# Optimization experiments

Hardware: AMD Instinct MI355X
Metric: run time of the kernel (lower is better)

Reference implementation:

```python
import jax, jax.numpy as jnp
import numpy as np

H = 64  # hidden size
T_ENC = 20
T_DEC = 30


def setup_inputs() -> dict:
    key = jax.random.key(0)
    ks = jax.random.split(key, 12)
    B = 65536
    s = 0.1
    return {
        "input_traj": jax.random.normal(ks[0], (B, T_ENC, 2), jnp.float32),
        "W_ih_enc": jax.random.normal(ks[1], (4 * H, 2), jnp.float32) * s,
        "W_hh_enc": jax.random.normal(ks[2], (4 * H, H), jnp.float32) * s,
        "b_ih_enc": jax.random.normal(ks[3], (4 * H,), jnp.float32) * s,
        "b_hh_enc": jax.random.normal(ks[4], (4 * H,), jnp.float32) * s,
        "W_ih_dec": jax.random.normal(ks[5], (4 * H, H), jnp.float32) * s,
        "W_hh_dec": jax.random.normal(ks[6], (4 * H, H), jnp.float32) * s,
        "b_ih_dec": jax.random.normal(ks[7], (4 * H,), jnp.float32) * s,
        "b_hh_dec": jax.random.normal(ks[8], (4 * H,), jnp.float32) * s,
        "W_emb": jax.random.normal(ks[9], (2, H), jnp.float32) * s,
        "b_emb": jax.random.normal(ks[10], (2,), jnp.float32) * s,
    }


def _lstm_cell(x, h, c, Wih, Whh, bih, bhh):
    # PyTorch LSTMCell gate order: i, f, g, o
    gates = x @ Wih.T + bih + h @ Whh.T + bhh  # [B, 4H]
    i, f, g, o = jnp.split(gates, 4, axis=-1)
    i = jax.nn.sigmoid(i)
    f = jax.nn.sigmoid(f)
    g = jnp.tanh(g)
    o = jax.nn.sigmoid(o)
    c_new = f * c + i * g
    h_new = o * jnp.tanh(c_new)
    return h_new, c_new


def reference(input_traj, W_ih_enc, W_hh_enc, b_ih_enc, b_hh_enc,
              W_ih_dec, W_hh_dec, b_ih_dec, b_hh_dec, W_emb, b_emb):
    B = input_traj.shape[0]
    h0 = jnp.zeros((B, H), input_traj.dtype)
    c0 = jnp.zeros((B, H), input_traj.dtype)

    # Encoder: scan over 20 timesteps (time-major inputs)
    xs = jnp.transpose(input_traj, (1, 0, 2))  # [T_ENC, B, 2]

    def enc_step(carry, x_t):
        h, c = carry
        h, c = _lstm_cell(x_t, h, c, W_ih_enc, W_hh_enc, b_ih_enc, b_hh_enc)
        return (h, c), None

    (h, c), _ = jax.lax.scan(enc_step, (h0, c0), xs)

    # Decoder: 30 steps, input at each step is the current hidden state
    def dec_step(carry, _):
        h, c = carry
        h, c = _lstm_cell(h, h, c, W_ih_dec, W_hh_dec, b_ih_dec, b_hh_dec)
        pos = h @ W_emb.T + b_emb  # [B, 2]
        return (h, c), pos

    (_, _), pos_seq = jax.lax.scan(dec_step, (h, c), None, length=T_DEC)
    pred_traj = jnp.transpose(pos_seq, (1, 0, 2))  # [B, T_DEC, 2]
    return pred_traj
```

## Files before the change

kernel.cpp:

```cpp
#include <hip/hip_runtime.h>

#define T_ENC 20
#define T_DEC 30
#define WAVES 4
#define EPB (WAVES * 32)

typedef __attribute__((ext_vector_type(8))) short short8;
typedef __attribute__((ext_vector_type(16))) float f32x16;

#if __has_builtin(__builtin_amdgcn_exp2f)
#define EXP2F(x) __builtin_amdgcn_exp2f(x)
#else
#define EXP2F(x) exp2f(x)
#endif
#if __has_builtin(__builtin_amdgcn_rcpf)
#define RCPF(x) __builtin_amdgcn_rcpf(x)
#else
#define RCPF(x) (1.0f / (x))
#endif

__device__ __forceinline__ float fast_sigmoid(float x) {
  float e = EXP2F(-1.4426950408889634f * x);
  return RCPF(1.0f + e);
}
__device__ __forceinline__ float fast_tanh(float x) {
  float e = EXP2F(2.8853900817779268f * x);
  return 1.0f - 2.0f * RCPF(e + 1.0f);
}

__device__ __forceinline__ unsigned short f2bf(float f) {
  unsigned u = __float_as_uint(f);
  u += 0x7fffu + ((u >> 16) & 1u);
  return (unsigned short)(u >> 16);
}
__device__ __forceinline__ float bf2f(unsigned short b) {
  return __uint_as_float(((unsigned)b) << 16);
}

#define MFMA32(a, b, c) __builtin_amdgcn_mfma_f32_32x32x16_bf16(a, b, c, 0, 0, 0)

__global__ __launch_bounds__(256, 1)
void SinglePrediction_88493506167138_kernel(
    const float* __restrict__ x,
    const float* __restrict__ W_ih_enc,
    const float* __restrict__ W_hh_enc,
    const float* __restrict__ b_ih_enc,
    const float* __restrict__ b_hh_enc,
    const float* __restrict__ W_ih_dec,
    const float* __restrict__ W_hh_dec,
    const float* __restrict__ b_ih_dec,
    const float* __restrict__ b_hh_dec,
    const float* __restrict__ W_emb,
    const float* __restrict__ b_emb,
    float* __restrict__ out)
{
  __shared__ __align__(16) unsigned short Wbf[2][256 * 64];
  __shared__ __align__(16) unsigned short hT[WAVES][2][32 * 64];
  __shared__ __align__(16) float xlds[WAVES][32][T_ENC * 2];
  __shared__ float bsum_l[256];

  const int tid = threadIdx.x;
  const int lane = tid & 63;
  const int wid = tid >> 6;
  const int hi5 = lane >> 5;
  const int l31 = lane & 31;
  const int beb = blockIdx.x * EPB;

  {
    const float4* src = (const float4*)(x + (size_t)beb * (T_ENC * 2));
    float4* dst = (float4*)&xlds[0][0][0];
    for (int i = tid; i < EPB * T_ENC * 2 / 4; i += 256) dst[i] = src[i];
  }
  for (int i = tid; i < 256 * 64; i += 256) {
    int row = i >> 6, k = i & 63;
    float w = W_hh_enc[i];
    unsigned short hb = f2bf(w);
    unsigned short lb = f2bf(w - bf2f(hb));
    int si = (row << 6) | (k ^ ((row & 7) << 3));
    Wbf[0][si] = hb;
    Wbf[1][si] = lb;
  }
  bsum_l[tid] = b_ih_enc[tid] + b_hh_enc[tid];
  {
    float4 z = {0.f, 0.f, 0.f, 0.f};
    float4* p = (float4*)&hT[wid][0][0];
    for (int i = lane; i < 512; i += 64) p[i] = z;
  }
  __syncthreads();

  float biasv[8], wi0[8], wi1[8];
#pragma unroll
  for (int nt = 0; nt < 8; nt++) {
    int n = nt * 32 + l31;
    biasv[nt] = bsum_l[n];
    float2 wv = *(const float2*)&W_ih_enc[2 * n];
    wi0[nt] = wv.x;
    wi1[nt] = wv.y;
  }

  float c01[2][16];
#pragma unroll
  for (int p = 0; p < 2; p++)
#pragma unroll
    for (int q = 0; q < 16; q++) c01[p][q] = 0.f;

  const int sw = (l31 & 7) << 3;
  const int kbase = hi5 << 3;

#pragma unroll 1
  for (int t = 0; t < T_ENC; t++) {
    short8 ah[4], al[4];
#pragma unroll
    for (int kt = 0; kt < 4; kt++) {
      int sk = (kt * 16 + kbase) ^ sw;
      ah[kt] = *(const short8*)&hT[wid][0][(l31 << 6) + sk];
      al[kt] = *(const short8*)&hT[wid][1][(l31 << 6) + sk];
    }
    float2 xr[16];
#pragma unroll
    for (int q = 0; q < 16; q++) {
      int row = (q & 3) + 8 * (q >> 2) + 4 * hi5;
      xr[q] = *(const float2*)&xlds[wid][row][2 * t];
    }
    f32x16 acc[8];
#pragma unroll
    for (int nt = 0; nt < 8; nt++)
#pragma unroll
      for (int q = 0; q < 16; q++)
        acc[nt][q] = fmaf(xr[q].x, wi0[nt], fmaf(xr[q].y, wi1[nt], biasv[nt]));
#pragma unroll
    for (int kt = 0; kt < 4; kt++) {
      short8 bh[8], bl[8];
      int sk = (kt * 16 + kbase) ^ sw;
#pragma unroll
      for (int nt = 0; nt < 8; nt++) {
        int r = nt * 32 + l31;
        bh[nt] = *(const short8*)&Wbf[0][(r << 6) + sk];
        bl[nt] = *(const short8*)&Wbf[1][(r << 6) + sk];
      }
#pragma unroll
      for (int nt = 0; nt < 8; nt++) acc[nt] = MFMA32(ah[kt], bh[nt], acc[nt]);
#pragma unroll
      for (int nt = 0; nt < 8; nt++) acc[nt] = MFMA32(al[kt], bh[nt], acc[nt]);
#pragma unroll
      for (int nt = 0; nt < 8; nt++) acc[nt] = MFMA32(ah[kt], bl[nt], acc[nt]);
    }
#pragma unroll
    for (int p = 0; p < 2; p++)
#pragma unroll
      for (int q = 0; q < 16; q++) {
        float ig = fast_sigmoid(acc[0 + p][q]);
        float fg = fast_sigmoid(acc[2 + p][q]);
        float gg = fast_tanh(acc[4 + p][q]);
        float og = fast_sigmoid(acc[6 + p][q]);
        float cn = fmaf(fg, c01[p][q], ig * gg);
        c01[p][q] = cn;
        float hn = og * fast_tanh(cn);
        unsigned short hb = f2bf(hn);
        unsigned short lb = f2bf(hn - bf2f(hb));
        int row = (q & 3) + 8 * (q >> 2) + 4 * hi5;
        int col = l31 + 32 * p;
        int si = (row << 6) | (col ^ ((row & 7) << 3));
        hT[wid][0][si] = hb;
        hT[wid][1][si] = lb;
      }
  }

  __syncthreads();
  for (int i = tid; i < 256 * 64; i += 256) {
    int row = i >> 6, k = i & 63;
    float w = W_ih_dec[i] + W_hh_dec[i];
    unsigned short hb = f2bf(w);
    unsigned short lb = f2bf(w - bf2f(hb));
    int si = (row << 6) | (k ^ ((row & 7) << 3));
    Wbf[0][si] = hb;
    Wbf[1][si] = lb;
  }
  bsum_l[tid] = b_ih_dec[tid] + b_hh_dec[tid];
  __syncthreads();

#pragma unroll
  for (int nt = 0; nt < 8; nt++) biasv[nt] = bsum_l[nt * 32 + l31];
  const float we00 = W_emb[l31];
  const float we01 = W_emb[32 + l31];
  const float we10 = W_emb[64 + l31];
  const float we11 = W_emb[96 + l31];
  const float be0 = b_emb[0];
  const float be1 = b_emb[1];

#pragma unroll 1
  for (int t = 0; t < T_DEC; t++) {
    short8 ah[4], al[4];
#pragma unroll
    for (int kt = 0; kt < 4; kt++) {
      int sk = (kt * 16 + kbase) ^ sw;
      ah[kt] = *(const short8*)&hT[wid][0][(l31 << 6) + sk];
      al[kt] = *(const short8*)&hT[wid][1][(l31 << 6) + sk];
    }
    f32x16 acc[8];
#pragma unroll
    for (int nt = 0; nt < 8; nt++)
#pragma unroll
      for (int q = 0; q < 16; q++) acc[nt][q] = biasv[nt];
#pragma unroll
    for (int kt = 0; kt < 4; kt++) {
      short8 bh[8], bl[8];
      int sk = (kt * 16 + kbase) ^ sw;
#pragma unroll
      for (int nt = 0; nt < 8; nt++) {
        int r = nt * 32 + l31;
        bh[nt] = *(const short8*)&Wbf[0][(r << 6) + sk];
        bl[nt] = *(const short8*)&Wbf[1][(r << 6) + sk];
      }
#pragma unroll
      for (int nt = 0; nt < 8; nt++) acc[nt] = MFMA32(ah[kt], bh[nt], acc[nt]);
#pragma unroll
      for (int nt = 0; nt < 8; nt++) acc[nt] = MFMA32(al[kt], bh[nt], acc[nt]);
#pragma unroll
      for (int nt = 0; nt < 8; nt++) acc[nt] = MFMA32(ah[kt], bl[nt], acc[nt]);
    }
    float hs[2][16];
#pragma unroll
    for (int p = 0; p < 2; p++)
#pragma unroll
      for (int q = 0; q < 16; q++) {
        float ig = fast_sigmoid(acc[0 + p][q]);
        float fg = fast_sigmoid(acc[2 + p][q]);
        float gg = fast_tanh(acc[4 + p][q]);
        float og = fast_sigmoid(acc[6 + p][q]);
        float cn = fmaf(fg, c01[p][q], ig * gg);
        c01[p][q] = cn;
        float hn = og * fast_tanh(cn);
        hs[p][q] = hn;
        unsigned short hb = f2bf(hn);
        unsigned short lb = f2bf(hn - bf2f(hb));
        int row = (q & 3) + 8 * (q >> 2) + 4 * hi5;
        int col = l31 + 32 * p;
        int si = (row << 6) | (col ^ ((row & 7) << 3));
        hT[wid][0][si] = hb;
        hT[wid][1][si] = lb;
      }
#pragma unroll
    for (int q = 0; q < 16; q++) {
      float p0 = fmaf(hs[0][q], we00, hs[1][q] * we01);
      float p1 = fmaf(hs[0][q], we10, hs[1][q] * we11);
#pragma unroll
      for (int m = 16; m >= 1; m >>= 1) {
        p0 += __shfl_xor(p0, m, 64);
        p1 += __shfl_xor(p1, m, 64);
      }
      if (l31 == 0) {
        int row = (q & 3) + 8 * (q >> 2) + 4 * hi5;
        float2 v;
        v.x = p0 + be0;
        v.y = p1 + be1;
        *(float2*)&out[(size_t)(beb + wid * 32 + row) * 60 + 2 * t] = v;
      }
    }
  }
}

extern "C" void kernel_launch(void* const* d_in, const int* in_sizes, int n_in,
                              void* d_out, int out_size, void* d_ws, size_t ws_size,
                              hipStream_t stream) {
  const float* x        = (const float*)d_in[0];
  const float* W_ih_enc = (const float*)d_in[1];
  const float* W_hh_enc = (const float*)d_in[2];
  const float* b_ih_enc = (const float*)d_in[3];
  const float* b_hh_enc = (const float*)d_in[4];
  const float* W_ih_dec = (const float*)d_in[5];
  const float* W_hh_dec = (const float*)d_in[6];
  const float* b_ih_dec = (const float*)d_in[7];
  const float* b_hh_dec = (const float*)d_in[8];
  const float* W_emb    = (const float*)d_in[9];
  const float* b_emb    = (const float*)d_in[10];
  float* out = (float*)d_out;

  const int B = in_sizes[0] / (T_ENC * 2);
  const int grid = B / EPB;

  hipLaunchKernelGGL(SinglePrediction_88493506167138_kernel,
                     dim3(grid), dim3(256), 0, stream,
                     x, W_ih_enc, W_hh_enc, b_ih_enc, b_hh_enc,
                     W_ih_dec, W_hh_dec, b_ih_dec, b_hh_dec,
                     W_emb, b_emb, out);
}
```

Before: 736.0 us.

## Use 8 waves per block, pre-scale gate weights, and compute embedding via MFMA

Doubles the waves per block so more batch tiles share one LDS copy of the weights. Gate weights and biases are pre-scaled by log2e factors to remove multiplies in the activations, and bf16 hi/lo splitting uses truncation. The output embedding is computed with an extra MFMA tile appended to the weight matrix, deferred one step, replacing shuffle reductions. Input trajectories are read directly from global memory instead of staged in LDS, which risks added latency and register pressure at 512 threads.

Result: slower. 1.785 ms (+142.5%).

```diff
diff --git a/kernel.cpp b/kernel.cpp
--- a/kernel.cpp
+++ b/kernel.cpp
@@ -2,7 +2,7 @@
 
 #define T_ENC 20
 #define T_DEC 30
-#define WAVES 4
+#define WAVES 8
 #define EPB (WAVES * 32)
 
 typedef __attribute__((ext_vector_type(8))) short short8;
@@ -19,27 +19,12 @@
 #define RCPF(x) (1.0f / (x))
 #endif
 
-__device__ __forceinline__ float fast_sigmoid(float x) {
-  float e = EXP2F(-1.4426950408889634f * x);
-  return RCPF(1.0f + e);
-}
-__device__ __forceinline__ float fast_tanh(float x) {
-  float e = EXP2F(2.8853900817779268f * x);
-  return 1.0f - 2.0f * RCPF(e + 1.0f);
-}
-
-__device__ __forceinline__ unsigned short f2bf(float f) {
-  unsigned u = __float_as_uint(f);
-  u += 0x7fffu + ((u >> 16) & 1u);
-  return (unsigned short)(u >> 16);
-}
-__device__ __forceinline__ float bf2f(unsigned short b) {
-  return __uint_as_float(((unsigned)b) << 16);
-}
+#define LOG2E 1.4426950408889634f
+#define TWO_LOG2E 2.8853900817779268f
 
 #define MFMA32(a, b, c) __builtin_amdgcn_mfma_f32_32x32x16_bf16(a, b, c, 0, 0, 0)
 
-__global__ __launch_bounds__(256, 1)
+__global__ __launch_bounds__(512, 2)
 void SinglePrediction_88493506167138_kernel(
     const float* __restrict__ x,
     const float* __restrict__ W_ih_enc,
@@ -54,9 +39,9 @@
     const float* __restrict__ b_emb,
     float* __restrict__ out)
 {
-  __shared__ __align__(16) unsigned short Wbf[2][256 * 64];
+  __shared__ __align__(16) unsigned short Wh[288 * 64];
+  __shared__ __align__(16) unsigned short Wl[288 * 64];
   __shared__ __align__(16) unsigned short hT[WAVES][2][32 * 64];
-  __shared__ __align__(16) float xlds[WAVES][32][T_ENC * 2];
   __shared__ float bsum_l[256];
 
   const int tid = threadIdx.x;
@@ -66,21 +51,20 @@
   const int l31 = lane & 31;
   const int beb = blockIdx.x * EPB;
 
-  {
-    const float4* src = (const float4*)(x + (size_t)beb * (T_ENC * 2));
-    float4* dst = (float4*)&xlds[0][0][0];
-    for (int i = tid; i < EPB * T_ENC * 2 / 4; i += 256) dst[i] = src[i];
-  }
-  for (int i = tid; i < 256 * 64; i += 256) {
+  for (int i = tid; i < 256 * 64; i += 512) {
     int row = i >> 6, k = i & 63;
-    float w = W_hh_enc[i];
-    unsigned short hb = f2bf(w);
-    unsigned short lb = f2bf(w - bf2f(hb));
+    float sc = ((row >> 6) == 2) ? TWO_LOG2E : LOG2E;
+    float w = W_hh_enc[i] * sc;
+    unsigned u = __float_as_uint(w);
+    float lo = w - __uint_as_float(u & 0xffff0000u);
     int si = (row << 6) | (k ^ ((row & 7) << 3));
-    Wbf[0][si] = hb;
-    Wbf[1][si] = lb;
-  }
-  bsum_l[tid] = b_ih_enc[tid] + b_hh_enc[tid];
+    Wh[si] = (unsigned short)(u >> 16);
+    Wl[si] = (unsigned short)(__float_as_uint(lo) >> 16);
+  }
+  if (tid < 256) {
+    float sc = ((tid >> 6) == 2) ? TWO_LOG2E : LOG2E;
+    bsum_l[tid] = (b_ih_enc[tid] + b_hh_enc[tid]) * sc;
+  }
   {
     float4 z = {0.f, 0.f, 0.f, 0.f};
     float4* p = (float4*)&hT[wid][0][0];
@@ -92,10 +76,11 @@
 #pragma unroll
   for (int nt = 0; nt < 8; nt++) {
     int n = nt * 32 + l31;
+    float sc = ((n >> 6) == 2) ? TWO_LOG2E : LOG2E;
     biasv[nt] = bsum_l[n];
     float2 wv = *(const float2*)&W_ih_enc[2 * n];
-    wi0[nt] = wv.x;
-    wi1[nt] = wv.y;
+    wi0[nt] = wv.x * sc;
+    wi1[nt] = wv.y * sc;
   }
 
   float c01[2][16];
@@ -107,27 +92,17 @@
   const int sw = (l31 & 7) << 3;
   const int kbase = hi5 << 3;
 
-#pragma unroll 1
-  for (int t = 0; t < T_ENC; t++) {
-    short8 ah[4], al[4];
+  short8 ah[4], al[4];
+  auto loadA = [&]() {
 #pragma unroll
     for (int kt = 0; kt < 4; kt++) {
       int sk = (kt * 16 + kbase) ^ sw;
       ah[kt] = *(const short8*)&hT[wid][0][(l31 << 6) + sk];
       al[kt] = *(const short8*)&hT[wid][1][(l31 << 6) + sk];
     }
-    float2 xr[16];
-#pragma unroll
-    for (int q = 0; q < 16; q++) {
-      int row = (q & 3) + 8 * (q >> 2) + 4 * hi5;
-      xr[q] = *(const float2*)&xlds[wid][row][2 * t];
-    }
-    f32x16 acc[8];
-#pragma unroll
-    for (int nt = 0; nt < 8; nt++)
-#pragma unroll
-      for (int q = 0; q < 16; q++)
-        acc[nt][q] = fmaf(xr[q].x, wi0[nt], fmaf(xr[q].y, wi1[nt], biasv[nt]));
+  };
+
+  auto gemm_main = [&](f32x16 (&acc)[8]) {
 #pragma unroll
     for (int kt = 0; kt < 4; kt++) {
       short8 bh[8], bl[8];
@@ -135,8 +110,8 @@
 #pragma unroll
       for (int nt = 0; nt < 8; nt++) {
         int r = nt * 32 + l31;
-        bh[nt] = *(const short8*)&Wbf[0][(r << 6) + sk];
-        bl[nt] = *(const short8*)&Wbf[1][(r << 6) + sk];
+        bh[nt] = *(const short8*)&Wh[(r << 6) + sk];
+        bl[nt] = *(const short8*)&Wl[(r << 6) + sk];
       }
 #pragma unroll
       for (int nt = 0; nt < 8; nt++) acc[nt] = MFMA32(ah[kt], bh[nt], acc[nt]);
@@ -145,119 +120,129 @@
 #pragma unroll
       for (int nt = 0; nt < 8; nt++) acc[nt] = MFMA32(ah[kt], bl[nt], acc[nt]);
     }
+  };
+
+  auto cell_update = [&](float gi, float gf, float gg_, float go, float& cc,
+                         int si_) {
+    float ig = RCPF(1.f + EXP2F(-gi));
+    float fg = RCPF(1.f + EXP2F(-gf));
+    float eg = EXP2F(gg_);
+    float gg = 1.f - 2.f * RCPF(eg + 1.f);
+    float og = RCPF(1.f + EXP2F(-go));
+    float cn = fmaf(fg, cc, ig * gg);
+    cc = cn;
+    float ec = EXP2F(TWO_LOG2E * cn);
+    float th = 1.f - 2.f * RCPF(ec + 1.f);
+    float hn = og * th;
+    unsigned u = __float_as_uint(hn);
+    float lo = hn - __uint_as_float(u & 0xffff0000u);
+    hT[wid][0][si_] = (unsigned short)(u >> 16);
+    hT[wid][1][si_] = (unsigned short)(__float_as_uint(lo) >> 16);
+  };
+
+#pragma unroll 1
+  for (int t = 0; t < T_ENC; t++) {
+    loadA();
+    float2 xr[16];
+#pragma unroll
+    for (int q = 0; q < 16; q++) {
+      int row = (q & 3) + 8 * (q >> 2) + 4 * hi5;
+      xr[q] = *(const float2*)&x[((size_t)(beb + wid * 32 + row)) * 40 + 2 * t];
+    }
+    f32x16 acc[8];
+#pragma unroll
+    for (int nt = 0; nt < 8; nt++)
+#pragma unroll
+      for (int q = 0; q < 16; q++)
+        acc[nt][q] = fmaf(xr[q].x, wi0[nt], fmaf(xr[q].y, wi1[nt], biasv[nt]));
+    gemm_main(acc);
 #pragma unroll
     for (int p = 0; p < 2; p++)
 #pragma unroll
       for (int q = 0; q < 16; q++) {
-        float ig = fast_sigmoid(acc[0 + p][q]);
-        float fg = fast_sigmoid(acc[2 + p][q]);
-        float gg = fast_tanh(acc[4 + p][q]);
-        float og = fast_sigmoid(acc[6 + p][q]);
-        float cn = fmaf(fg, c01[p][q], ig * gg);
-        c01[p][q] = cn;
-        float hn = og * fast_tanh(cn);
-        unsigned short hb = f2bf(hn);
-        unsigned short lb = f2bf(hn - bf2f(hb));
         int row = (q & 3) + 8 * (q >> 2) + 4 * hi5;
         int col = l31 + 32 * p;
         int si = (row << 6) | (col ^ ((row & 7) << 3));
-        hT[wid][0][si] = hb;
-        hT[wid][1][si] = lb;
+        cell_update(acc[0 + p][q], acc[2 + p][q], acc[4 + p][q], acc[6 + p][q],
+                    c01[p][q], si);
       }
   }
 
   __syncthreads();
-  for (int i = tid; i < 256 * 64; i += 256) {
+  for (int i = tid; i < 288 * 64; i += 512) {
     int row = i >> 6, k = i & 63;
-    float w = W_ih_dec[i] + W_hh_dec[i];
-    unsigned short hb = f2bf(w);
-    unsigned short lb = f2bf(w - bf2f(hb));
+    float w;
+    if (row < 256) {
+      float sc = ((row >> 6) == 2) ? TWO_LOG2E : LOG2E;
+      w = (W_ih_dec[i] + W_hh_dec[i]) * sc;
+    } else if (row < 258) {
+      w = W_emb[(row - 256) * 64 + k];
+    } else {
+      w = 0.f;
+    }
+    unsigned u = __float_as_uint(w);
+    float lo = w - __uint_as_float(u & 0xffff0000u);
     int si = (row << 6) | (k ^ ((row & 7) << 3));
-    Wbf[0][si] = hb;
-    Wbf[1][si] = lb;
-  }
-  bsum_l[tid] = b_ih_dec[tid] + b_hh_dec[tid];
+    Wh[si] = (unsigned short)(u >> 16);
+    Wl[si] = (unsigned short)(__float_as_uint(lo) >> 16);
+  }
+  if (tid < 256) {
+    float sc = ((tid >> 6) == 2) ? TWO_LOG2E : LOG2E;
+    bsum_l[tid] = (b_ih_dec[tid] + b_hh_dec[tid]) * sc;
+  }
   __syncthreads();
 
 #pragma unroll
   for (int nt = 0; nt < 8; nt++) biasv[nt] = bsum_l[nt * 32 + l31];
-  const float we00 = W_emb[l31];
-  const float we01 = W_emb[32 + l31];
-  const float we10 = W_emb[64 + l31];
-  const float we11 = W_emb[96 + l31];
-  const float be0 = b_emb[0];
-  const float be1 = b_emb[1];
+  const float bev = (l31 == 0) ? b_emb[0] : b_emb[1];
+
+  auto do_pos = [&](int tout) {
+    f32x16 accP;
+#pragma unroll
+    for (int q = 0; q < 16; q++) accP[q] = 0.f;
+#pragma unroll
+    for (int kt = 0; kt < 4; kt++) {
+      int sk = (kt * 16 + kbase) ^ sw;
+      int r = 256 + l31;
+      short8 beh = *(const short8*)&Wh[(r << 6) + sk];
+      short8 bel = *(const short8*)&Wl[(r << 6) + sk];
+      accP = MFMA32(ah[kt], beh, accP);
+      accP = MFMA32(al[kt], beh, accP);
+      accP = MFMA32(ah[kt], bel, accP);
+    }
+    if (l31 < 2) {
+#pragma unroll
+      for (int q = 0; q < 16; q++) {
+        int row = (q & 3) + 8 * (q >> 2) + 4 * hi5;
+        out[(size_t)(beb + wid * 32 + row) * 60 + 2 * tout + l31] =
+            accP[q] + bev;
+      }
+    }
+  };
 
 #pragma unroll 1
   for (int t = 0; t < T_DEC; t++) {
-    short8 ah[4], al[4];
-#pragma unroll
-    for (int kt = 0; kt < 4; kt++) {
-      int sk = (kt * 16 + kbase) ^ sw;
-      ah[kt] = *(const short8*)&hT[wid][0][(l31 << 6) + sk];
-      al[kt] = *(const short8*)&hT[wid][1][(l31 << 6) + sk];
-    }
+    loadA();
+    if (t > 0) do_pos(t - 1);
     f32x16 acc[8];
 #pragma unroll
     for (int nt = 0; nt < 8; nt++)
 #pragma unroll
       for (int q = 0; q < 16; q++) acc[nt][q] = biasv[nt];
-#pragma unroll
-    for (int kt = 0; kt < 4; kt++) {
-      short8 bh[8], bl[8];
-      int sk = (kt * 16 + kbase) ^ sw;
-#pragma unroll
-      for (int nt = 0; nt < 8; nt++) {
-        int r = nt * 32 + l31;
-        bh[nt] = *(const short8*)&Wbf[0][(r << 6) + sk];
-        bl[nt] = *(const short8*)&Wbf[1][(r << 6) + sk];
-      }
-#pragma unroll
-      for (int nt = 0; nt < 8; nt++) acc[nt] = MFMA32(ah[kt], bh[nt], acc[nt]);
-#pragma unroll
-      for (int nt = 0; nt < 8; nt++) acc[nt] = MFMA32(al[kt], bh[nt], acc[nt]);
-#pragma unroll
-      for (int nt = 0; nt < 8; nt++) acc[nt] = MFMA32(ah[kt], bl[nt], acc[nt]);
-    }
-    float hs[2][16];
+    gemm_main(acc);
 #pragma unroll
     for (int p = 0; p < 2; p++)
 #pragma unroll
       for (int q = 0; q < 16; q++) {
-        float ig = fast_sigmoid(acc[0 + p][q]);
-        float fg = fast_sigmoid(acc[2 + p][q]);
-        float gg = fast_tanh(acc[4 + p][q]);
-        float og = fast_sigmoid(acc[6 + p][q]);
-        float cn = fmaf(fg, c01[p][q], ig * gg);
-        c01[p][q] = cn;
-        float hn = og * fast_tanh(cn);
-        hs[p][q] = hn;
-        unsigned short hb = f2bf(hn);
-        unsigned short lb = f2bf(hn - bf2f(hb));
         int row = (q & 3) + 8 * (q >> 2) + 4 * hi5;
         int col = l31 + 32 * p;
         int si = (row << 6) | (col ^ ((row & 7) << 3));
-        hT[wid][0][si] = hb;
-        hT[wid][1][si] = lb;
-      }
-#pragma unroll
-    for (int q = 0; q < 16; q++) {
-      float p0 = fmaf(hs[0][q], we00, hs[1][q] * we01);
-      float p1 = fmaf(hs[0][q], we10, hs[1][q] * we11);
-#pragma unroll
-      for (int m = 16; m >= 1; m >>= 1) {
-        p0 += __shfl_xor(p0, m, 64);
-        p1 += __shfl_xor(p1, m, 64);
-      }
-      if (l31 == 0) {
-        int row = (q & 3) + 8 * (q >> 2) + 4 * hi5;
-        float2 v;
-        v.x = p0 + be0;
-        v.y = p1 + be1;
-        *(float2*)&out[(size_t)(beb + wid * 32 + row) * 60 + 2 * t] = v;
-      }
-    }
-  }
+        cell_update(acc[0 + p][q], acc[2 + p][q], acc[4 + p][q], acc[6 + p][q],
+                    c01[p][q], si);
+      }
+  }
+  loadA();
+  do_pos(T_DEC - 1);
 }
 
 extern "C" void kernel_launch(void* const* d_in, const int* in_sizes, int n_in,
@@ -280,7 +265,7 @@
   const int grid = B / EPB;
 
   hipLaunchKernelGGL(SinglePrediction_88493506167138_kernel,
-                     dim3(grid), dim3(256), 0, stream,
+                     dim3(grid), dim3(512), 0, stream,
                      x, W_ih_enc, W_hh_enc, b_ih_enc, b_hh_enc,
                      W_ih_dec, W_hh_dec, b_ih_dec, b_hh_dec,
                      W_emb, b_emb, out);
```
